# Optimization experiments

Measured on AMD Instinct MI355X. Metric: run time of the kernel, lower is better.

Reference implementation:

```python
import jax, jax.numpy as jnp
import numpy as np

H_BINS = 64
SIGMA = 0.02
EPS = 1e-6


def setup_inputs() -> dict:
    key = jax.random.key(0)
    x = jax.random.uniform(key, (8, 3, 256, 256), dtype=jnp.float32)
    return {"x": x}


def reference(x):
    h = H_BINS
    L = x.shape[0]
    x = jnp.clip(x, 0.0, 1.0)
    I = x.reshape(L, 3, -1)                      # [L,3,N]
    Iy = jnp.sqrt(jnp.sum(I * I, axis=1) + EPS)  # [L,N] pixel intensity
    logs = jnp.log(I + EPS)                      # [L,3,N]
    # per-channel log-chromaticity: for c=0:(u=l0-l1, v=l0-l2); c=1:(l1-l0, l1-l2); c=2:(l2-l0, l2-l1)
    cu = jnp.array([1, 0, 0])
    cv = jnp.array([2, 2, 1])
    U = logs - logs[:, cu, :]                    # [L,3,N]
    V = logs - logs[:, cv, :]                    # [L,3,N]
    offset = jnp.linspace(-3.0, 3.0, h, dtype=jnp.float32)  # [h]
    inv_s2 = jnp.float32(1.0 / (SIGMA * SIGMA))
    # RBF-like (inverse-quadratic) soft binning kernels: [L,3,N,h]
    Ku = 1.0 / (1.0 + jnp.square(U[..., None] - offset) * inv_s2)
    Kv = 1.0 / (1.0 + jnp.square(V[..., None] - offset) * inv_s2)
    # weighted outer-product reduction over pixels -> [L,3,h,h]
    hists = jnp.einsum('ln,lcnu,lcnv->lcuv', Iy, Ku, Kv)
    # normalize each sample by its total mass
    total = jnp.sum(hists, axis=(1, 2, 3), keepdims=True)
    return hists / (total + EPS)
```

## Files before the change

### kernel.cpp

```cpp
#include <hip/hip_runtime.h>

#define H 64
#define NPIX 65536
#define LBATCH 8
#define LC 24
#define S_CHUNKS 32
#define PB 2048
#define EPSF 1e-6f
#define LN2_50 34.6573590f
#define NPART (LC * S_CHUNKS)
#define PART_FLOATS (NPART * H * H)

typedef _Float16 h8 __attribute__((ext_vector_type(8)));
typedef __fp16   g2 __attribute__((ext_vector_type(2)));
typedef float f32x16 __attribute__((ext_vector_type(16)));
union H8u { h8 v8; g2 v2[4]; };

#define PK(a, b) __builtin_amdgcn_cvt_pkrtz((a), (b))

#define KEV4(k0, k1, k2, k3, d0, d1, d2, d3) { \
    const float q0 = fmaf((d0), (d0), 1.0f); \
    const float q1 = fmaf((d1), (d1), 1.0f); \
    const float q2 = fmaf((d2), (d2), 1.0f); \
    const float q3 = fmaf((d3), (d3), 1.0f); \
    const float p01 = q0 * q1, p23 = q2 * q3; \
    const float r = __builtin_amdgcn_rcpf(p01 * p23); \
    const float r23 = p23 * r, r01 = p01 * r; \
    k0 = q1 * r23; k1 = q0 * r23; k2 = q3 * r01; k3 = q2 * r01; }

__global__ __launch_bounds__(256, 3) void hist_main(const float* __restrict__ x,
                                                    float* __restrict__ ws) {
    __shared__ float sU[PB];
    __shared__ float sV[PB];
    __shared__ float sW[PB];
    __shared__ float sHist[H * H];

    const int tid  = threadIdx.x;
    const int wv   = tid >> 6;
    const int lane = tid & 63;
    const int hf   = lane >> 5;
    const int ln   = lane & 31;
    const int lc   = blockIdx.y;
    const int l    = lc / 3;
    const int c    = lc - 3 * l;

    #pragma unroll
    for (int r = 0; r < 4; r++)
        *(float4*)&sHist[(r * 256 + tid) * 4] = make_float4(0.f, 0.f, 0.f, 0.f);

    const float* __restrict__ x0p = x + (l * 3 + 0) * NPIX;
    const float* __restrict__ x1p = x + (l * 3 + 1) * NPIX;
    const float* __restrict__ x2p = x + (l * 3 + 2) * NPIX;
    const int base = blockIdx.x * PB;

    #pragma unroll
    for (int pass = 0; pass < 2; pass++) {
        const int ploc = pass * 1024 + tid * 4;
        const float4 r0 = *(const float4*)&x0p[base + ploc];
        const float4 r1 = *(const float4*)&x1p[base + ploc];
        const float4 r2 = *(const float4*)&x2p[base + ploc];
        float4 U4, V4, W4;
        #define PREP(E) { \
            const float v0 = fminf(fmaxf(r0.E, 0.0f), 1.0f); \
            const float v1 = fminf(fmaxf(r1.E, 0.0f), 1.0f); \
            const float v2 = fminf(fmaxf(r2.E, 0.0f), 1.0f); \
            W4.E = __builtin_amdgcn_sqrtf(fmaf(v0, v0, fmaf(v1, v1, fmaf(v2, v2, EPSF)))); \
            const float lg0 = __builtin_amdgcn_logf(v0 + EPSF); \
            const float lg1 = __builtin_amdgcn_logf(v1 + EPSF); \
            const float lg2 = __builtin_amdgcn_logf(v2 + EPSF); \
            float U, V; \
            if (c == 0)      { U = lg0 - lg1; V = lg0 - lg2; } \
            else if (c == 1) { U = lg1 - lg0; V = lg1 - lg2; } \
            else             { U = lg2 - lg0; V = lg2 - lg1; } \
            U4.E = LN2_50 * U; V4.E = LN2_50 * V; }
        PREP(x) PREP(y) PREP(z) PREP(w)
        #undef PREP
        *(float4*)&sU[ploc] = U4;
        *(float4*)&sV[ploc] = V4;
        *(float4*)&sW[ploc] = W4;
    }
    __syncthreads();

    const float step50 = 50.0f * (6.0f / 63.0f);
    const float ou0 = -150.0f + step50 * (float)ln;
    const float ou1 = ou0 + step50 * 32.0f;

    f32x16 acc00, acc01, acc10, acc11;
    #pragma unroll
    for (int i = 0; i < 16; i++) { acc00[i] = 0.f; acc01[i] = 0.f; acc10[i] = 0.f; acc11[i] = 0.f; }

    const int wbase = wv * 512;
    #pragma unroll 2
    for (int ks = 0; ks < 32; ks++) {
        const int kb = wbase + ks * 16 + hf * 8;
        const float4 ua = *(const float4*)&sU[kb];
        const float4 ub = *(const float4*)&sU[kb + 4];
        const float4 va = *(const float4*)&sV[kb];
        const float4 vb = *(const float4*)&sV[kb + 4];
        const float4 wa = *(const float4*)&sW[kb];
        const float4 wb = *(const float4*)&sW[kb + 4];
        H8u A0, A1, B0, B1;
        float k0, k1, k2, k3;
        KEV4(k0, k1, k2, k3, ua.x - ou0, ua.y - ou0, ua.z - ou0, ua.w - ou0)
        A0.v2[0] = PK(wa.x * k0, wa.y * k1);
        A0.v2[1] = PK(wa.z * k2, wa.w * k3);
        KEV4(k0, k1, k2, k3, ub.x - ou0, ub.y - ou0, ub.z - ou0, ub.w - ou0)
        A0.v2[2] = PK(wb.x * k0, wb.y * k1);
        A0.v2[3] = PK(wb.z * k2, wb.w * k3);
        KEV4(k0, k1, k2, k3, ua.x - ou1, ua.y - ou1, ua.z - ou1, ua.w - ou1)
        A1.v2[0] = PK(wa.x * k0, wa.y * k1);
        A1.v2[1] = PK(wa.z * k2, wa.w * k3);
        KEV4(k0, k1, k2, k3, ub.x - ou1, ub.y - ou1, ub.z - ou1, ub.w - ou1)
        A1.v2[2] = PK(wb.x * k0, wb.y * k1);
        A1.v2[3] = PK(wb.z * k2, wb.w * k3);
        KEV4(k0, k1, k2, k3, va.x - ou0, va.y - ou0, va.z - ou0, va.w - ou0)
        B0.v2[0] = PK(k0, k1);
        B0.v2[1] = PK(k2, k3);
        KEV4(k0, k1, k2, k3, vb.x - ou0, vb.y - ou0, vb.z - ou0, vb.w - ou0)
        B0.v2[2] = PK(k0, k1);
        B0.v2[3] = PK(k2, k3);
        KEV4(k0, k1, k2, k3, va.x - ou1, va.y - ou1, va.z - ou1, va.w - ou1)
        B1.v2[0] = PK(k0, k1);
        B1.v2[1] = PK(k2, k3);
        KEV4(k0, k1, k2, k3, vb.x - ou1, vb.y - ou1, vb.z - ou1, vb.w - ou1)
        B1.v2[2] = PK(k0, k1);
        B1.v2[3] = PK(k2, k3);
        acc00 = __builtin_amdgcn_mfma_f32_32x32x16_f16(A0.v8, B0.v8, acc00, 0, 0, 0);
        acc01 = __builtin_amdgcn_mfma_f32_32x32x16_f16(A0.v8, B1.v8, acc01, 0, 0, 0);
        acc10 = __builtin_amdgcn_mfma_f32_32x32x16_f16(A1.v8, B0.v8, acc10, 0, 0, 0);
        acc11 = __builtin_amdgcn_mfma_f32_32x32x16_f16(A1.v8, B1.v8, acc11, 0, 0, 0);
    }

    #pragma unroll
    for (int r = 0; r < 16; r++) {
        const int row = (r & 3) + 8 * (r >> 2) + 4 * hf;
        atomicAdd(&sHist[row * 64 + ln],             acc00[r]);
        atomicAdd(&sHist[row * 64 + 32 + ln],        acc01[r]);
        atomicAdd(&sHist[(row + 32) * 64 + ln],      acc10[r]);
        atomicAdd(&sHist[(row + 32) * 64 + 32 + ln], acc11[r]);
    }
    __syncthreads();

    float* __restrict__ g = ws + (lc * S_CHUNKS + blockIdx.x) * (H * H);
    #pragma unroll
    for (int r = 0; r < 4; r++) {
        const int i = (r * 256 + tid) * 4;
        *(float4*)&g[i] = *(const float4*)&sHist[i];
    }
}

__global__ __launch_bounds__(256) void hist_reduce(const float* __restrict__ ws,
                                                   float* __restrict__ out,
                                                   float* __restrict__ wsq) {
    const int lc  = blockIdx.x >> 2;
    const int off = (blockIdx.x & 3) * 1024 + threadIdx.x * 4;
    float4 a = make_float4(0.f, 0.f, 0.f, 0.f);
    #pragma unroll 8
    for (int ch = 0; ch < S_CHUNKS; ch++) {
        const float4 v = *(const float4*)&ws[(lc * S_CHUNKS + ch) * (H * H) + off];
        a.x += v.x; a.y += v.y; a.z += v.z; a.w += v.w;
    }
    *(float4*)&out[lc * (H * H) + off] = a;

    float s = (a.x + a.y) + (a.z + a.w);
    #pragma unroll
    for (int o = 32; o > 0; o >>= 1) s += __shfl_down(s, o, 64);
    __shared__ float ps[4];
    if ((threadIdx.x & 63) == 0) ps[threadIdx.x >> 6] = s;
    __syncthreads();
    if (threadIdx.x == 0) wsq[blockIdx.x] = (ps[0] + ps[1]) + (ps[2] + ps[3]);
}

__global__ __launch_bounds__(256) void hist_scale(float* __restrict__ out,
                                                  const float* __restrict__ wsq) {
    const int lc = blockIdx.x >> 2;
    const int l  = lc / 3;
    float T = 0.f;
    #pragma unroll
    for (int j = 0; j < 12; j++) T += wsq[l * 12 + j];
    const float inv = 1.0f / (T + EPSF);
    const int off = (blockIdx.x & 3) * 1024 + threadIdx.x * 4;
    float4 v = *(const float4*)&out[lc * (H * H) + off];
    v.x *= inv; v.y *= inv; v.z *= inv; v.w *= inv;
    *(float4*)&out[lc * (H * H) + off] = v;
}

extern "C" void kernel_launch(void* const* d_in, const int* in_sizes, int n_in,
                              void* d_out, int out_size, void* d_ws, size_t ws_size,
                              hipStream_t stream) {
    const float* x = (const float*)d_in[0];
    float* out = (float*)d_out;
    float* ws = (float*)d_ws;

    hipLaunchKernelGGL(hist_main,   dim3(S_CHUNKS, LC), dim3(256), 0, stream, x, ws);
    hipLaunchKernelGGL(hist_reduce, dim3(96),           dim3(256), 0, stream, ws, out, ws + PART_FLOATS);
    hipLaunchKernelGGL(hist_scale,  dim3(96),           dim3(256), 0, stream, out, ws + PART_FLOATS);
}
```

Baseline: 157.1 us.

## Use 1024-thread blocks over fewer chunks with staged LDS passes

```diff
diff --git a/kernel.cpp b/kernel.cpp
--- a/kernel.cpp
+++ b/kernel.cpp
@@ -4,11 +4,12 @@
 #define NPIX 65536
 #define LBATCH 8
 #define LC 24
-#define S_CHUNKS 32
-#define PB 2048
+#define NCH 8
+#define PBT 8192
+#define SP 2048
 #define EPSF 1e-6f
 #define LN2_50 34.6573590f
-#define NPART (LC * S_CHUNKS)
+#define NPART (LC * NCH)
 #define PART_FLOATS (NPART * H * H)
 
 typedef _Float16 h8 __attribute__((ext_vector_type(8)));
@@ -28,11 +29,11 @@
     const float r23 = p23 * r, r01 = p01 * r; \
     k0 = q1 * r23; k1 = q0 * r23; k2 = q3 * r01; k3 = q2 * r01; }
 
-__global__ __launch_bounds__(256, 3) void hist_main(const float* __restrict__ x,
-                                                    float* __restrict__ ws) {
-    __shared__ float sU[PB];
-    __shared__ float sV[PB];
-    __shared__ float sW[PB];
+__global__ __launch_bounds__(1024, 4) void hist_main(const float* __restrict__ x,
+                                                     float* __restrict__ ws) {
+    __shared__ float sU[SP];
+    __shared__ float sV[SP];
+    __shared__ float sW[SP];
     __shared__ float sHist[H * H];
 
     const int tid  = threadIdx.x;
@@ -44,42 +45,12 @@
     const int l    = lc / 3;
     const int c    = lc - 3 * l;
 
-    #pragma unroll
-    for (int r = 0; r < 4; r++)
-        *(float4*)&sHist[(r * 256 + tid) * 4] = make_float4(0.f, 0.f, 0.f, 0.f);
+    *(float4*)&sHist[tid * 4] = make_float4(0.f, 0.f, 0.f, 0.f);
 
     const float* __restrict__ x0p = x + (l * 3 + 0) * NPIX;
     const float* __restrict__ x1p = x + (l * 3 + 1) * NPIX;
     const float* __restrict__ x2p = x + (l * 3 + 2) * NPIX;
-    const int base = blockIdx.x * PB;
-
-    #pragma unroll
-    for (int pass = 0; pass < 2; pass++) {
-        const int ploc = pass * 1024 + tid * 4;
-        const float4 r0 = *(const float4*)&x0p[base + ploc];
-        const float4 r1 = *(const float4*)&x1p[base + ploc];
-        const float4 r2 = *(const float4*)&x2p[base + ploc];
-        float4 U4, V4, W4;
-        #define PREP(E) { \
-            const float v0 = fminf(fmaxf(r0.E, 0.0f), 1.0f); \
-            const float v1 = fminf(fmaxf(r1.E, 0.0f), 1.0f); \
-            const float v2 = fminf(fmaxf(r2.E, 0.0f), 1.0f); \
-            W4.E = __builtin_amdgcn_sqrtf(fmaf(v0, v0, fmaf(v1, v1, fmaf(v2, v2, EPSF)))); \
-            const float lg0 = __builtin_amdgcn_logf(v0 + EPSF); \
-            const float lg1 = __builtin_amdgcn_logf(v1 + EPSF); \
-            const float lg2 = __builtin_amdgcn_logf(v2 + EPSF); \
-            float U, V; \
-            if (c == 0)      { U = lg0 - lg1; V = lg0 - lg2; } \
-            else if (c == 1) { U = lg1 - lg0; V = lg1 - lg2; } \
-            else             { U = lg2 - lg0; V = lg2 - lg1; } \
-            U4.E = LN2_50 * U; V4.E = LN2_50 * V; }
-        PREP(x) PREP(y) PREP(z) PREP(w)
-        #undef PREP
-        *(float4*)&sU[ploc] = U4;
-        *(float4*)&sV[ploc] = V4;
-        *(float4*)&sW[ploc] = W4;
-    }
-    __syncthreads();
+    const int base = blockIdx.x * PBT;
 
     const float step50 = 50.0f * (6.0f / 63.0f);
     const float ou0 = -150.0f + step50 * (float)ln;
@@ -89,46 +60,78 @@
     #pragma unroll
     for (int i = 0; i < 16; i++) { acc00[i] = 0.f; acc01[i] = 0.f; acc10[i] = 0.f; acc11[i] = 0.f; }
 
-    const int wbase = wv * 512;
-    #pragma unroll 2
-    for (int ks = 0; ks < 32; ks++) {
-        const int kb = wbase + ks * 16 + hf * 8;
-        const float4 ua = *(const float4*)&sU[kb];
-        const float4 ub = *(const float4*)&sU[kb + 4];
-        const float4 va = *(const float4*)&sV[kb];
-        const float4 vb = *(const float4*)&sV[kb + 4];
-        const float4 wa = *(const float4*)&sW[kb];
-        const float4 wb = *(const float4*)&sW[kb + 4];
-        H8u A0, A1, B0, B1;
-        float k0, k1, k2, k3;
-        KEV4(k0, k1, k2, k3, ua.x - ou0, ua.y - ou0, ua.z - ou0, ua.w - ou0)
-        A0.v2[0] = PK(wa.x * k0, wa.y * k1);
-        A0.v2[1] = PK(wa.z * k2, wa.w * k3);
-        KEV4(k0, k1, k2, k3, ub.x - ou0, ub.y - ou0, ub.z - ou0, ub.w - ou0)
-        A0.v2[2] = PK(wb.x * k0, wb.y * k1);
-        A0.v2[3] = PK(wb.z * k2, wb.w * k3);
-        KEV4(k0, k1, k2, k3, ua.x - ou1, ua.y - ou1, ua.z - ou1, ua.w - ou1)
-        A1.v2[0] = PK(wa.x * k0, wa.y * k1);
-        A1.v2[1] = PK(wa.z * k2, wa.w * k3);
-        KEV4(k0, k1, k2, k3, ub.x - ou1, ub.y - ou1, ub.z - ou1, ub.w - ou1)
-        A1.v2[2] = PK(wb.x * k0, wb.y * k1);
-        A1.v2[3] = PK(wb.z * k2, wb.w * k3);
-        KEV4(k0, k1, k2, k3, va.x - ou0, va.y - ou0, va.z - ou0, va.w - ou0)
-        B0.v2[0] = PK(k0, k1);
-        B0.v2[1] = PK(k2, k3);
-        KEV4(k0, k1, k2, k3, vb.x - ou0, vb.y - ou0, vb.z - ou0, vb.w - ou0)
-        B0.v2[2] = PK(k0, k1);
-        B0.v2[3] = PK(k2, k3);
-        KEV4(k0, k1, k2, k3, va.x - ou1, va.y - ou1, va.z - ou1, va.w - ou1)
-        B1.v2[0] = PK(k0, k1);
-        B1.v2[1] = PK(k2, k3);
-        KEV4(k0, k1, k2, k3, vb.x - ou1, vb.y - ou1, vb.z - ou1, vb.w - ou1)
-        B1.v2[2] = PK(k0, k1);
-        B1.v2[3] = PK(k2, k3);
-        acc00 = __builtin_amdgcn_mfma_f32_32x32x16_f16(A0.v8, B0.v8, acc00, 0, 0, 0);
-        acc01 = __builtin_amdgcn_mfma_f32_32x32x16_f16(A0.v8, B1.v8, acc01, 0, 0, 0);
-        acc10 = __builtin_amdgcn_mfma_f32_32x32x16_f16(A1.v8, B0.v8, acc10, 0, 0, 0);
-        acc11 = __builtin_amdgcn_mfma_f32_32x32x16_f16(A1.v8, B1.v8, acc11, 0, 0, 0);
+    const int wbase = wv * (SP / 16);
+
+    for (int pass = 0; pass < PBT / SP; pass++) {
+        {
+            const int ploc = tid * 2;
+            const int gp = base + pass * SP + ploc;
+            const float2 r0 = *(const float2*)&x0p[gp];
+            const float2 r1 = *(const float2*)&x1p[gp];
+            const float2 r2 = *(const float2*)&x2p[gp];
+            float2 U2, V2, W2;
+            #define PREP(E) { \
+                const float v0 = fminf(fmaxf(r0.E, 0.0f), 1.0f); \
+                const float v1 = fminf(fmaxf(r1.E, 0.0f), 1.0f); \
+                const float v2 = fminf(fmaxf(r2.E, 0.0f), 1.0f); \
+                W2.E = __builtin_amdgcn_sqrtf(fmaf(v0, v0, fmaf(v1, v1, fmaf(v2, v2, EPSF)))); \
+                const float lg0 = __builtin_amdgcn_logf(v0 + EPSF); \
+                const float lg1 = __builtin_amdgcn_logf(v1 + EPSF); \
+                const float lg2 = __builtin_amdgcn_logf(v2 + EPSF); \
+                float U, V; \
+                if (c == 0)      { U = lg0 - lg1; V = lg0 - lg2; } \
+                else if (c == 1) { U = lg1 - lg0; V = lg1 - lg2; } \
+                else             { U = lg2 - lg0; V = lg2 - lg1; } \
+                U2.E = LN2_50 * U; V2.E = LN2_50 * V; }
+            PREP(x) PREP(y)
+            #undef PREP
+            *(float2*)&sU[ploc] = U2;
+            *(float2*)&sV[ploc] = V2;
+            *(float2*)&sW[ploc] = W2;
+        }
+        __syncthreads();
+
+        #pragma unroll 2
+        for (int ks = 0; ks < SP / 16 / 16; ks++) {
+            const int kb = wbase + ks * 16 + hf * 8;
+            const float4 ua = *(const float4*)&sU[kb];
+            const float4 ub = *(const float4*)&sU[kb + 4];
+            const float4 va = *(const float4*)&sV[kb];
+            const float4 vb = *(const float4*)&sV[kb + 4];
+            const float4 wa = *(const float4*)&sW[kb];
+            const float4 wb = *(const float4*)&sW[kb + 4];
+            H8u A0, A1, B0, B1;
+            float k0, k1, k2, k3;
+            KEV4(k0, k1, k2, k3, ua.x - ou0, ua.y - ou0, ua.z - ou0, ua.w - ou0)
+            A0.v2[0] = PK(wa.x * k0, wa.y * k1);
+            A0.v2[1] = PK(wa.z * k2, wa.w * k3);
+            KEV4(k0, k1, k2, k3, ub.x - ou0, ub.y - ou0, ub.z - ou0, ub.w - ou0)
+            A0.v2[2] = PK(wb.x * k0, wb.y * k1);
+            A0.v2[3] = PK(wb.z * k2, wb.w * k3);
+            KEV4(k0, k1, k2, k3, ua.x - ou1, ua.y - ou1, ua.z - ou1, ua.w - ou1)
+            A1.v2[0] = PK(wa.x * k0, wa.y * k1);
+            A1.v2[1] = PK(wa.z * k2, wa.w * k3);
+            KEV4(k0, k1, k2, k3, ub.x - ou1, ub.y - ou1, ub.z - ou1, ub.w - ou1)
+            A1.v2[2] = PK(wb.x * k0, wb.y * k1);
+            A1.v2[3] = PK(wb.z * k2, wb.w * k3);
+            KEV4(k0, k1, k2, k3, va.x - ou0, va.y - ou0, va.z - ou0, va.w - ou0)
+            B0.v2[0] = PK(k0, k1);
+            B0.v2[1] = PK(k2, k3);
+            KEV4(k0, k1, k2, k3, vb.x - ou0, vb.y - ou0, vb.z - ou0, vb.w - ou0)
+            B0.v2[2] = PK(k0, k1);
+            B0.v2[3] = PK(k2, k3);
+            KEV4(k0, k1, k2, k3, va.x - ou1, va.y - ou1, va.z - ou1, va.w - ou1)
+            B1.v2[0] = PK(k0, k1);
+            B1.v2[1] = PK(k2, k3);
+            KEV4(k0, k1, k2, k3, vb.x - ou1, vb.y - ou1, vb.z - ou1, vb.w - ou1)
+            B1.v2[2] = PK(k0, k1);
+            B1.v2[3] = PK(k2, k3);
+            acc00 = __builtin_amdgcn_mfma_f32_32x32x16_f16(A0.v8, B0.v8, acc00, 0, 0, 0);
+            acc01 = __builtin_amdgcn_mfma_f32_32x32x16_f16(A0.v8, B1.v8, acc01, 0, 0, 0);
+            acc10 = __builtin_amdgcn_mfma_f32_32x32x16_f16(A1.v8, B0.v8, acc10, 0, 0, 0);
+            acc11 = __builtin_amdgcn_mfma_f32_32x32x16_f16(A1.v8, B1.v8, acc11, 0, 0, 0);
+        }
+        __syncthreads();
     }
 
     #pragma unroll
@@ -141,12 +144,8 @@
     }
     __syncthreads();
 
-    float* __restrict__ g = ws + (lc * S_CHUNKS + blockIdx.x) * (H * H);
-    #pragma unroll
-    for (int r = 0; r < 4; r++) {
-        const int i = (r * 256 + tid) * 4;
-        *(float4*)&g[i] = *(const float4*)&sHist[i];
-    }
+    float* __restrict__ g = ws + (lc * NCH + blockIdx.x) * (H * H);
+    *(float4*)&g[tid * 4] = *(const float4*)&sHist[tid * 4];
 }
 
 __global__ __launch_bounds__(256) void hist_reduce(const float* __restrict__ ws,
@@ -155,9 +154,9 @@
     const int lc  = blockIdx.x >> 2;
     const int off = (blockIdx.x & 3) * 1024 + threadIdx.x * 4;
     float4 a = make_float4(0.f, 0.f, 0.f, 0.f);
-    #pragma unroll 8
-    for (int ch = 0; ch < S_CHUNKS; ch++) {
-        const float4 v = *(const float4*)&ws[(lc * S_CHUNKS + ch) * (H * H) + off];
+    #pragma unroll
+    for (int ch = 0; ch < NCH; ch++) {
+        const float4 v = *(const float4*)&ws[(lc * NCH + ch) * (H * H) + off];
         a.x += v.x; a.y += v.y; a.z += v.z; a.w += v.w;
     }
     *(float4*)&out[lc * (H * H) + off] = a;
@@ -192,7 +191,7 @@
     float* out = (float*)d_out;
     float* ws = (float*)d_ws;
 
-    hipLaunchKernelGGL(hist_main,   dim3(S_CHUNKS, LC), dim3(256), 0, stream, x, ws);
-    hipLaunchKernelGGL(hist_reduce, dim3(96),           dim3(256), 0, stream, ws, out, ws + PART_FLOATS);
-    hipLaunchKernelGGL(hist_scale,  dim3(96),           dim3(256), 0, stream, out, ws + PART_FLOATS);
+    hipLaunchKernelGGL(hist_main,   dim3(NCH, LC), dim3(1024), 0, stream, x, ws);
+    hipLaunchKernelGGL(hist_reduce, dim3(96),      dim3(256),  0, stream, ws, out, ws + PART_FLOATS);
+    hipLaunchKernelGGL(hist_scale,  dim3(96),      dim3(256),  0, stream, out, ws + PART_FLOATS);
 }
```

Result: slower. 189.5 us (+20.6%).

## Fuse histogram, reduce and scale into one cooperative kernel with grid syncs

Applied to the files above, without the earlier changes.

```diff
diff --git a/kernel.cpp b/kernel.cpp
--- a/kernel.cpp
+++ b/kernel.cpp
@@ -1,4 +1,7 @@
 #include <hip/hip_runtime.h>
+#include <hip/hip_cooperative_groups.h>
+
+namespace cg = cooperative_groups;
 
 #define H 64
 #define NPIX 65536
@@ -28,13 +31,10 @@
     const float r23 = p23 * r, r01 = p01 * r; \
     k0 = q1 * r23; k1 = q0 * r23; k2 = q3 * r01; k3 = q2 * r01; }
 
-__global__ __launch_bounds__(256, 3) void hist_main(const float* __restrict__ x,
-                                                    float* __restrict__ ws) {
-    __shared__ float sU[PB];
-    __shared__ float sV[PB];
-    __shared__ float sW[PB];
-    __shared__ float sHist[H * H];
-
+__device__ __forceinline__ void phaseA(const float* __restrict__ x,
+                                       float* __restrict__ ws,
+                                       float* sU, float* sV, float* sW,
+                                       float* sHist) {
     const int tid  = threadIdx.x;
     const int wv   = tid >> 6;
     const int lane = tid & 63;
@@ -149,6 +149,68 @@
     }
 }
 
+__global__ __launch_bounds__(256, 3) void hist_fused(const float* __restrict__ x,
+                                                     float* __restrict__ out,
+                                                     float* __restrict__ ws) {
+    __shared__ float sU[PB];
+    __shared__ float sV[PB];
+    __shared__ float sW[PB];
+    __shared__ float sHist[H * H];
+
+    phaseA(x, ws, sU, sV, sW, sHist);
+
+    __threadfence();
+    cg::this_grid().sync();
+
+    const int flat = blockIdx.y * gridDim.x + blockIdx.x;
+    float* __restrict__ wsq = ws + PART_FLOATS;
+
+    if (flat < 96) {
+        const int lc  = flat >> 2;
+        const int off = (flat & 3) * 1024 + threadIdx.x * 4;
+        float4 a = make_float4(0.f, 0.f, 0.f, 0.f);
+        #pragma unroll 8
+        for (int ch = 0; ch < S_CHUNKS; ch++) {
+            const float4 v = *(const float4*)&ws[(lc * S_CHUNKS + ch) * (H * H) + off];
+            a.x += v.x; a.y += v.y; a.z += v.z; a.w += v.w;
+        }
+        *(float4*)&out[lc * (H * H) + off] = a;
+
+        float s = (a.x + a.y) + (a.z + a.w);
+        #pragma unroll
+        for (int o = 32; o > 0; o >>= 1) s += __shfl_down(s, o, 64);
+        float* ps = sHist;
+        if ((threadIdx.x & 63) == 0) ps[threadIdx.x >> 6] = s;
+        __syncthreads();
+        if (threadIdx.x == 0) wsq[flat] = (ps[0] + ps[1]) + (ps[2] + ps[3]);
+    }
+
+    __threadfence();
+    cg::this_grid().sync();
+
+    if (flat < 96) {
+        const int lc = flat >> 2;
+        const int l  = lc / 3;
+        float T = 0.f;
+        #pragma unroll
+        for (int j = 0; j < 12; j++) T += wsq[l * 12 + j];
+        const float inv = 1.0f / (T + EPSF);
+        const int off = (flat & 3) * 1024 + threadIdx.x * 4;
+        float4 v = *(const float4*)&out[lc * (H * H) + off];
+        v.x *= inv; v.y *= inv; v.z *= inv; v.w *= inv;
+        *(float4*)&out[lc * (H * H) + off] = v;
+    }
+}
+
+__global__ __launch_bounds__(256, 3) void hist_mainF(const float* __restrict__ x,
+                                                     float* __restrict__ ws) {
+    __shared__ float sU[PB];
+    __shared__ float sV[PB];
+    __shared__ float sW[PB];
+    __shared__ float sHist[H * H];
+    phaseA(x, ws, sU, sV, sW, sHist);
+}
+
 __global__ __launch_bounds__(256) void hist_reduce(const float* __restrict__ ws,
                                                    float* __restrict__ out,
                                                    float* __restrict__ wsq) {
@@ -192,7 +254,13 @@
     float* out = (float*)d_out;
     float* ws = (float*)d_ws;
 
-    hipLaunchKernelGGL(hist_main,   dim3(S_CHUNKS, LC), dim3(256), 0, stream, x, ws);
-    hipLaunchKernelGGL(hist_reduce, dim3(96),           dim3(256), 0, stream, ws, out, ws + PART_FLOATS);
-    hipLaunchKernelGGL(hist_scale,  dim3(96),           dim3(256), 0, stream, out, ws + PART_FLOATS);
-}
+    void* args[] = {(void*)&x, (void*)&out, (void*)&ws};
+    hipError_t err = hipLaunchCooperativeKernel((const void*)hist_fused,
+                                                dim3(S_CHUNKS, LC), dim3(256),
+                                                args, 0, stream);
+    if (err != hipSuccess) {
+        hipLaunchKernelGGL(hist_mainF,  dim3(S_CHUNKS, LC), dim3(256), 0, stream, x, ws);
+        hipLaunchKernelGGL(hist_reduce, dim3(96),           dim3(256), 0, stream, ws, out, ws + PART_FLOATS);
+        hipLaunchKernelGGL(hist_scale,  dim3(96),           dim3(256), 0, stream, out, ws + PART_FLOATS);
+    }
+}
```

Result: slower. 383.4 us (+144.1%).
